# Kernel optimization log

Measured on AMD Instinct MI355X. Metric: run time of the kernel, lower is better.

The kernel has to match this reference:

```python
import jax, jax.numpy as jnp
import numpy as np

# --- config (Qwen3-Next linear attention defaults) ---
B, S, H = 1, 256, 2048
NK, NV, DK, DV, K = 4, 32, 128, 128, 4
KEY_DIM = NK * DK          # 512
VAL_DIM = NV * DV          # 4096
CONV_DIM = 2 * KEY_DIM + VAL_DIM  # 5120
EPS = 1e-6


def setup_inputs() -> dict:
    key = jax.random.key(0)
    ks = jax.random.split(key, 8)
    rn = lambda k, shape, sc: jax.random.normal(k, shape, jnp.float32) * sc
    return {
        "hidden_states": jax.random.normal(ks[0], (B, S, H), jnp.float32),
        "w_qkvz": rn(ks[1], (2 * KEY_DIM + 2 * VAL_DIM, H), 0.02),  # in_proj_qkvz weight
        "w_ba": rn(ks[2], (2 * NV, H), 0.02),                        # in_proj_ba weight
        "w_out": rn(ks[3], (H, VAL_DIM), 0.02),                      # out_proj weight
        "conv_w": rn(ks[4], (CONV_DIM, 1, K), 0.1),                  # depthwise conv weight [C,1,K]
        "dt_bias": jnp.ones((NV,), jnp.float32),
        "A_log": jnp.zeros((NV,), jnp.float32),
        "norm_w": jnp.ones((DV,), jnp.float32),
    }


def reference(hidden_states, w_qkvz, w_ba, w_out, conv_w, dt_bias, A_log, norm_w):
    b, s, _ = hidden_states.shape
    # input projections (Linear without bias: x @ W.T)
    qkvz = hidden_states @ w_qkvz.T                      # [B,S,9216]
    ba = hidden_states @ w_ba.T                          # [B,S,64]
    q, k, v, z = jnp.split(qkvz, [KEY_DIM, 2 * KEY_DIM, 2 * KEY_DIM + VAL_DIM], axis=-1)
    beta, alpha = jnp.split(ba, 2, axis=-1)              # each [B,S,NV]

    # causal depthwise conv over concat(q,k,v), then silu
    qkv = jnp.concatenate([q, k, v], axis=-1).transpose(0, 2, 1)   # [B,C,S]
    qkv = jax.lax.conv_general_dilated(
        qkv, conv_w, window_strides=(1,), padding=[(K - 1, 0)],
        dimension_numbers=("NCH", "OIH", "NCH"), feature_group_count=CONV_DIM)
    qkv = jax.nn.silu(qkv).transpose(0, 2, 1)            # [B,S,C]
    q, k, v = jnp.split(qkv, [KEY_DIM, 2 * KEY_DIM], axis=-1)

    q = q.reshape(b, s, NK, DK)
    k = k.reshape(b, s, NK, DK)
    v = v.reshape(b, s, NV, DV)
    z = z.reshape(b, s, NV, DV)

    # GQA-style head expansion (repeat_interleave)
    ratio = NV // NK
    q = jnp.repeat(q, ratio, axis=2)                     # [B,S,NV,DK]
    k = jnp.repeat(k, ratio, axis=2)

    # NOTE: original computes g = -softplus(-A_log - alpha) but never uses it (dead code).
    beta_g = jax.nn.sigmoid(beta + dt_bias)[..., None]   # [B,S,NV,1]
    q = q * (DK ** -0.5)

    # naive delta-rule: full outer-product tensor + cumsum (memory-bound)
    kv = jnp.einsum("bsnk,bsnv->bsnkv", k, v * beta_g)   # [B,S,NV,DK,DV]
    out = jnp.einsum("bsnk,bsnkv->bsnv", q, jnp.cumsum(kv, axis=1))  # [B,S,NV,DV]

    # gated RMSNorm over head_v_dim in fp32
    of = out.astype(jnp.float32)
    var = jnp.mean(of * of, axis=-1, keepdims=True)
    of = of * jax.lax.rsqrt(var + EPS) * norm_w
    of = of * jax.nn.silu(z.astype(jnp.float32))

    return of.reshape(b, s, VAL_DIM) @ w_out.T           # [B,S,H]
```

## Files before the change

kernel.cpp:

```cpp
#include <hip/hip_runtime.h>
#include <hip/hip_bf16.h>

#define S_LEN   256
#define HID     2048
#define NVH     32
#define DKD     128
#define DVD     128
#define KEYDIM  512
#define VALDIM  4096
#define CONVDIM 5120
#define QKVZ_N  9216
#define EPS_F   1e-6f

typedef __attribute__((ext_vector_type(8))) short bf16x8;
typedef __attribute__((ext_vector_type(4))) float f32x4;

__device__ __forceinline__ unsigned short f2bf(float f) {
    union { float f; unsigned int i; } v; v.f = f;
    unsigned int x = v.i;
    return (unsigned short)((x + 0x7FFFu + ((x >> 16) & 1u)) >> 16);
}
__device__ __forceinline__ unsigned int pk2(float x, float y) {
    union { __hip_bfloat162 h; unsigned int u; } c;
    c.h = __float22bfloat162_rn(float2{x, y});
    return c.u;
}
__device__ __forceinline__ bf16x8 pack_bf8(float4 lo, float4 hi) {
    union { uint4 u; bf16x8 h; } c;
    c.u.x = pk2(lo.x, lo.y); c.u.y = pk2(lo.z, lo.w);
    c.u.z = pk2(hi.x, hi.y); c.u.w = pk2(hi.z, hi.w);
    return c.h;
}
__device__ __forceinline__ void gl_lds16(const void* g, void* l) {
    __builtin_amdgcn_global_load_lds(
        (const __attribute__((address_space(1))) unsigned int*)g,
        (__attribute__((address_space(3))) unsigned int*)l,
        16, 0, 0);
}

template<int NT>
__global__ __launch_bounds__(256, 3)
void gemm_sn(const unsigned short* __restrict__ A, const float* __restrict__ B,
             float* __restrict__ Cpart, int N, int K, int kc) {
    __shared__ __align__(16) unsigned short As[256][64];
    __shared__ __align__(16) float Bs[NT][64];

    const int tid  = threadIdx.x;
    const int lane = tid & 63, wave = tid >> 6;
    const int quad = lane >> 4, l16 = lane & 15;
    const int n0 = blockIdx.x * NT;
    const int kbeg = blockIdx.y * kc;
    const int niter = kc >> 6;
    constexpr int NB = NT / 16;

    const int a_ro = lane >> 3;
    const int a_gc = (lane & 7) ^ a_ro;
    const int b_ro = lane >> 4;
    const int b_cs = lane & 15;

    f32x4 acc[4][NB];
#pragma unroll
    for (int i = 0; i < 4; i++)
#pragma unroll
        for (int j = 0; j < NB; j++) acc[i][j] = (f32x4){0.f, 0.f, 0.f, 0.f};

    auto stage = [&](int kk) {
#pragma unroll
        for (int t = 0; t < 8; ++t) {
            int rbase = wave * 64 + t * 8;
            gl_lds16(A + (size_t)(rbase + a_ro) * K + kk + a_gc * 8,
                     &As[rbase][0]);
        }
#pragma unroll
        for (int t = 0; t < NT / 16; ++t) {
            int rbase = wave * (NT / 4) + t * 4;
            int r = rbase + b_ro;
            int gc = b_cs ^ (r & 7);
            gl_lds16(B + (size_t)(n0 + r) * K + kk + gc * 4,
                     &Bs[rbase][0]);
        }
    };

    auto compute = [&]() {
#pragma unroll
        for (int ks = 0; ks < 2; ++ks) {
            bf16x8 af[4];
#pragma unroll
            for (int i = 0; i < 4; ++i) {
                int r = wave * 64 + i * 16 + l16;
                int c = (ks * 4 + quad) ^ (l16 & 7);
                af[i] = *(const bf16x8*)(&As[r][c * 8]);
            }
#pragma unroll
            for (int j = 0; j < NB; ++j) {
                int r = j * 16 + l16;
                int x = l16 & 7;
                int c0 = (ks * 8 + quad * 2) ^ x;
                int c1 = (ks * 8 + quad * 2 + 1) ^ x;
                float4 lo = *(const float4*)(&Bs[r][c0 * 4]);
                float4 hi = *(const float4*)(&Bs[r][c1 * 4]);
                bf16x8 bfr = pack_bf8(lo, hi);
#pragma unroll
                for (int i = 0; i < 4; ++i)
                    acc[i][j] = __builtin_amdgcn_mfma_f32_16x16x32_bf16(af[i], bfr, acc[i][j], 0, 0, 0);
            }
        }
    };

    stage(kbeg);
    for (int it = 0; it < niter; ++it) {
        __syncthreads();
        compute();
        if (it + 1 < niter) {
            __syncthreads();
            stage(kbeg + (it + 1) * 64);
        }
    }

    float* C = Cpart + (size_t)blockIdx.y * 256 * N;
#pragma unroll
    for (int i = 0; i < 4; i++)
#pragma unroll
        for (int j = 0; j < NB; j++)
#pragma unroll
            for (int r = 0; r < 4; r++) {
                int row = wave * 64 + i * 16 + quad * 4 + r;
                int col = n0 + j * 16 + l16;
                C[(size_t)row * N + col] = acc[i][j][r];
            }
}

__global__ __launch_bounds__(256)
void cvt_bf16(const float* __restrict__ in, unsigned short* __restrict__ out, int n8) {
    int i = blockIdx.x * 256 + threadIdx.x;
    if (i >= n8) return;
    const float4* p = (const float4*)in + (size_t)i * 2;
    float4 a = p[0], b = p[1];
    uint4 r;
    r.x = pk2(a.x, a.y); r.y = pk2(a.z, a.w);
    r.z = pk2(b.x, b.y); r.w = pk2(b.z, b.w);
    *((uint4*)out + i) = r;
}

template<int P>
__global__ void reduce_sum(const float* __restrict__ part, float* __restrict__ out, int n) {
    int i = (blockIdx.x * 256 + threadIdx.x) * 4;
    if (i >= n) return;
    float4 s = *(const float4*)(part + i);
#pragma unroll
    for (int p = 1; p < P; p++) {
        float4 v = *(const float4*)(part + (size_t)p * n + i);
        s.x += v.x; s.y += v.y; s.z += v.z; s.w += v.w;
    }
    *(float4*)(out + i) = s;
}

__global__ __launch_bounds__(256)
void ba_proj(const float* __restrict__ hs,
             const float* __restrict__ w_ba,
             float* __restrict__ ba) {
    int s = blockIdx.x;
    int n = threadIdx.x & 63, seg = threadIdx.x >> 6;
    const float* x = hs + (size_t)s * HID + seg * 512;
    const float* w = w_ba + (size_t)n * HID + seg * 512;
    float acc = 0.f;
#pragma unroll 4
    for (int k = 0; k < 512; k += 4) {
        float4 xv = *(const float4*)(x + k);
        float4 wv = *(const float4*)(w + k);
        acc += xv.x * wv.x + xv.y * wv.y + xv.z * wv.z + xv.w * wv.w;
    }
    __shared__ float parts[4][64];
    parts[seg][n] = acc;
    __syncthreads();
    if (threadIdx.x < 64)
        ba[s * 64 + threadIdx.x] = parts[0][threadIdx.x] + parts[1][threadIdx.x]
                                 + parts[2][threadIdx.x] + parts[3][threadIdx.x];
}

__global__ void conv_silu(const float* __restrict__ qkvz,
                          const float* __restrict__ conv_w,
                          float* __restrict__ out) {
    int idx = blockIdx.x * blockDim.x + threadIdx.x;
    if (idx >= S_LEN * CONVDIM) return;
    int s = idx / CONVDIM, c = idx % CONVDIM;
    float acc = 0.f;
#pragma unroll
    for (int j = 0; j < 4; j++) {
        int t = s - 3 + j;
        if (t >= 0) acc += qkvz[(size_t)t * QKVZ_N + c] * conv_w[c * 4 + j];
    }
    out[idx] = acc / (1.f + __expf(-acc));
}

__global__ __launch_bounds__(256)
void scores_k(const float* __restrict__ conv, const float* __restrict__ ba,
              const float* __restrict__ dt_bias, float* __restrict__ scores) {
    if (blockIdx.x > blockIdx.y) return;
    int hk = blockIdx.z;
    int s0 = blockIdx.y * 16, t0 = blockIdx.x * 16;
    __shared__ float Qs[16][132], Ks[16][132];
    int tid = threadIdx.x;
    int qoff = hk * DKD;
    int koff = KEYDIM + hk * DKD;
    for (int idx = tid; idx < 16 * 128; idx += 256) {
        int i = idx >> 7, d = idx & 127;
        Qs[i][d] = conv[(size_t)(s0 + i) * CONVDIM + qoff + d];
        Ks[i][d] = conv[(size_t)(t0 + i) * CONVDIM + koff + d];
    }
    __syncthreads();
    int tx = tid & 15, ty = tid >> 4;
    int s = s0 + ty, t = t0 + tx;
    float dot = 0.f;
    for (int d = 0; d < 128; d++) dot += Qs[ty][d] * Ks[tx][d];
    float base = (t <= s) ? dot * 0.08838834764831845f : 0.f;
#pragma unroll
    for (int v = 0; v < 8; v++) {
        int n = hk * 8 + v;
        float b = ba[t * 64 + n] + dt_bias[n];
        float bg = 1.f / (1.f + __expf(-b));
        scores[((size_t)n * 256 + s) * 256 + t] = base * bg;
    }
}

__global__ __launch_bounds__(256)
void attn_v(const float* __restrict__ scores, const float* __restrict__ conv,
            float* __restrict__ attn) {
    int n = blockIdx.y, s0 = blockIdx.x * 16;
    int voff = 2 * KEYDIM + n * DVD;
    __shared__ float Ss[16][17];
    __shared__ float Vs[16][132];
    int tid = threadIdx.x, sy = tid >> 4, dx = tid & 15;
    float acc[8] = {0.f, 0.f, 0.f, 0.f, 0.f, 0.f, 0.f, 0.f};
    for (int t0 = 0; t0 <= s0; t0 += 16) {
        Ss[sy][dx] = scores[((size_t)n * 256 + s0 + sy) * 256 + t0 + dx];
        const float* vp = conv + (size_t)(t0 + sy) * CONVDIM + voff + dx * 8;
        *(float4*)&Vs[sy][dx * 8]     = *(const float4*)vp;
        *(float4*)&Vs[sy][dx * 8 + 4] = *(const float4*)(vp + 4);
        __syncthreads();
#pragma unroll
        for (int j = 0; j < 16; j++) {
            float sv = Ss[sy][j];
#pragma unroll
            for (int r = 0; r < 8; r++) acc[r] += sv * Vs[j][dx + 16 * r];
        }
        __syncthreads();
    }
    float* op = attn + ((size_t)(s0 + sy) * NVH + n) * DVD;
#pragma unroll
    for (int r = 0; r < 8; r++) op[dx + 16 * r] = acc[r];
}

__global__ __launch_bounds__(128)
void rmsnorm_gate(const float* __restrict__ attn, const float* __restrict__ qkvz,
                  const float* __restrict__ norm_w,
                  unsigned short* __restrict__ normed) {
    int s = blockIdx.x >> 5, n = blockIdx.x & 31;
    int d = threadIdx.x;
    float x = attn[((size_t)s * NVH + n) * DVD + d];
    float sq = x * x;
#pragma unroll
    for (int off = 32; off > 0; off >>= 1) sq += __shfl_down(sq, off, 64);
    __shared__ float parts[2];
    if ((d & 63) == 0) parts[d >> 6] = sq;
    __syncthreads();
    float ms = (parts[0] + parts[1]) * (1.f / 128.f);
    float inv = rsqrtf(ms + EPS_F);
    float z = qkvz[(size_t)s * QKVZ_N + CONVDIM + n * DVD + d];
    float sz = z / (1.f + __expf(-z));
    float v = x * inv * norm_w[d] * sz;
    normed[((size_t)s * NVH + n) * DVD + d] = f2bf(v);
}

extern "C" void kernel_launch(void* const* d_in, const int* in_sizes, int n_in,
                              void* d_out, int out_size, void* d_ws, size_t ws_size,
                              hipStream_t stream) {
    const float* hs      = (const float*)d_in[0];
    const float* w_qkvz  = (const float*)d_in[1];
    const float* w_ba    = (const float*)d_in[2];
    const float* w_out   = (const float*)d_in[3];
    const float* conv_w  = (const float*)d_in[4];
    const float* dt_bias = (const float*)d_in[5];
    const float* norm_w  = (const float*)d_in[7];

    char* ws = (char*)d_ws;
    float* qkvz = (float*)ws;  ws += (size_t)S_LEN * QKVZ_N * 4;
    float* ba   = (float*)ws;  ws += (size_t)S_LEN * 64 * 4;
    float* conv = (float*)ws;  ws += (size_t)S_LEN * CONVDIM * 4;
    unsigned short* abf = (unsigned short*)ws;
    ws += (size_t)S_LEN * HID * 2;
    char* regB = ws;
    float* scratch1 = (float*)regB;
    unsigned short* normed = (unsigned short*)regB;
    float* scratch2 = (float*)(regB + 2097152);
    float* attn   = (float*)(regB + 2097152);
    float* scores = (float*)(regB + 2097152 + 4194304);

    const bool big = ws_size >= (size_t)55 * 1024 * 1024;
    const int sk1 = big ? 4 : 2;

    cvt_bf16<<<(S_LEN * HID / 8) / 256, 256, 0, stream>>>(hs, abf, S_LEN * HID / 8);
    if (big) gemm_sn<64><<<dim3(QKVZ_N / 64, 4), 256, 0, stream>>>(abf, w_qkvz, scratch1, QKVZ_N, HID, HID / 4);
    else     gemm_sn<64><<<dim3(QKVZ_N / 64, 2), 256, 0, stream>>>(abf, w_qkvz, scratch1, QKVZ_N, HID, HID / 2);
    ba_proj<<<S_LEN, 256, 0, stream>>>(hs, w_ba, ba);
    if (big) reduce_sum<4><<<(S_LEN * QKVZ_N) / 1024, 256, 0, stream>>>(scratch1, qkvz, S_LEN * QKVZ_N);
    else     reduce_sum<2><<<(S_LEN * QKVZ_N) / 1024, 256, 0, stream>>>(scratch1, qkvz, S_LEN * QKVZ_N);
    conv_silu<<<(S_LEN * CONVDIM) / 256, 256, 0, stream>>>(qkvz, conv_w, conv);
    scores_k<<<dim3(16, 16, 4), 256, 0, stream>>>(conv, ba, dt_bias, scores);
    attn_v<<<dim3(16, NVH), 256, 0, stream>>>(scores, conv, attn);
    rmsnorm_gate<<<S_LEN * NVH, 128, 0, stream>>>(attn, qkvz, norm_w, normed);
    gemm_sn<32><<<dim3(HID / 32, 8), 256, 0, stream>>>(normed, w_out, scratch2, HID, VALDIM, VALDIM / 8);
    reduce_sum<8><<<(S_LEN * HID) / 1024, 256, 0, stream>>>(scratch2, (float*)d_out, S_LEN * HID);
}
```

Baseline: 256.6 us.

## Double-buffer GEMM with M tiling and fuse reduce/conv and attn/rmsnorm kernels

The GEMM is rewritten to split M into two 128-row tiles on a 2x2 wave grid. It double-buffers LDS so the next K chunk is staged while the current one is computed, with a single barrier per iteration. The bf16 conversion of hidden_states is fused into ba_proj, the split-K reduction is fused with the causal conv+silu (z is also written out separately), and RMSNorm gating is fused into the attention-V epilogue. The aim is fewer launches, fewer full-size intermediate round trips and better load/compute overlap. The cost is higher LDS use and lower occupancy, and the split-K and workspace layout now depend on a changed ws_size threshold.

```diff
diff --git a/kernel.cpp b/kernel.cpp
--- a/kernel.cpp
+++ b/kernel.cpp
@@ -39,37 +39,37 @@
 }
 
 template<int NT>
-__global__ __launch_bounds__(256, 3)
-void gemm_sn(const unsigned short* __restrict__ A, const float* __restrict__ B,
+__global__ __launch_bounds__(256, 2)
+void gemm_db(const unsigned short* __restrict__ A, const float* __restrict__ B,
              float* __restrict__ Cpart, int N, int K, int kc) {
-    __shared__ __align__(16) unsigned short As[256][64];
-    __shared__ __align__(16) float Bs[NT][64];
+    __shared__ __align__(16) unsigned short As[2][128][64];
+    __shared__ __align__(16) float Bs[2][NT][64];
 
     const int tid  = threadIdx.x;
     const int lane = tid & 63, wave = tid >> 6;
+    const int wm = wave >> 1, wn = wave & 1;
     const int quad = lane >> 4, l16 = lane & 15;
-    const int n0 = blockIdx.x * NT;
-    const int kbeg = blockIdx.y * kc;
+    const int m0 = blockIdx.y * 128, n0 = blockIdx.x * NT;
+    const int kbeg = blockIdx.z * kc;
     const int niter = kc >> 6;
-    constexpr int NB = NT / 16;
 
     const int a_ro = lane >> 3;
     const int a_gc = (lane & 7) ^ a_ro;
     const int b_ro = lane >> 4;
     const int b_cs = lane & 15;
 
-    f32x4 acc[4][NB];
+    f32x4 acc[4][2];
 #pragma unroll
     for (int i = 0; i < 4; i++)
 #pragma unroll
-        for (int j = 0; j < NB; j++) acc[i][j] = (f32x4){0.f, 0.f, 0.f, 0.f};
-
-    auto stage = [&](int kk) {
-#pragma unroll
-        for (int t = 0; t < 8; ++t) {
-            int rbase = wave * 64 + t * 8;
-            gl_lds16(A + (size_t)(rbase + a_ro) * K + kk + a_gc * 8,
-                     &As[rbase][0]);
+        for (int j = 0; j < 2; j++) acc[i][j] = (f32x4){0.f, 0.f, 0.f, 0.f};
+
+    auto stage = [&](int buf, int kk) {
+#pragma unroll
+        for (int t = 0; t < 4; ++t) {
+            int rbase = wave * 32 + t * 8;
+            gl_lds16(A + (size_t)(m0 + rbase + a_ro) * K + kk + a_gc * 8,
+                     &As[buf][rbase][0]);
         }
 #pragma unroll
         for (int t = 0; t < NT / 16; ++t) {
@@ -77,28 +77,28 @@
             int r = rbase + b_ro;
             int gc = b_cs ^ (r & 7);
             gl_lds16(B + (size_t)(n0 + r) * K + kk + gc * 4,
-                     &Bs[rbase][0]);
+                     &Bs[buf][rbase][0]);
         }
     };
 
-    auto compute = [&]() {
+    auto compute = [&](int buf) {
 #pragma unroll
         for (int ks = 0; ks < 2; ++ks) {
             bf16x8 af[4];
 #pragma unroll
             for (int i = 0; i < 4; ++i) {
-                int r = wave * 64 + i * 16 + l16;
+                int r = wm * 64 + i * 16 + l16;
                 int c = (ks * 4 + quad) ^ (l16 & 7);
-                af[i] = *(const bf16x8*)(&As[r][c * 8]);
+                af[i] = *(const bf16x8*)(&As[buf][r][c * 8]);
             }
 #pragma unroll
-            for (int j = 0; j < NB; ++j) {
-                int r = j * 16 + l16;
+            for (int j = 0; j < 2; ++j) {
+                int r = wn * 32 + j * 16 + l16;
                 int x = l16 & 7;
                 int c0 = (ks * 8 + quad * 2) ^ x;
                 int c1 = (ks * 8 + quad * 2 + 1) ^ x;
-                float4 lo = *(const float4*)(&Bs[r][c0 * 4]);
-                float4 hi = *(const float4*)(&Bs[r][c1 * 4]);
+                float4 lo = *(const float4*)(&Bs[buf][r][c0 * 4]);
+                float4 hi = *(const float4*)(&Bs[buf][r][c1 * 4]);
                 bf16x8 bfr = pack_bf8(lo, hi);
 #pragma unroll
                 for (int i = 0; i < 4; ++i)
@@ -107,39 +107,25 @@
         }
     };
 
-    stage(kbeg);
+    stage(0, kbeg);
+    __syncthreads();
     for (int it = 0; it < niter; ++it) {
+        if (it + 1 < niter) stage((it + 1) & 1, kbeg + (it + 1) * 64);
+        compute(it & 1);
         __syncthreads();
-        compute();
-        if (it + 1 < niter) {
-            __syncthreads();
-            stage(kbeg + (it + 1) * 64);
-        }
-    }
-
-    float* C = Cpart + (size_t)blockIdx.y * 256 * N;
+    }
+
+    float* C = Cpart + (size_t)blockIdx.z * 256 * N;
 #pragma unroll
     for (int i = 0; i < 4; i++)
 #pragma unroll
-        for (int j = 0; j < NB; j++)
+        for (int j = 0; j < 2; j++)
 #pragma unroll
             for (int r = 0; r < 4; r++) {
-                int row = wave * 64 + i * 16 + quad * 4 + r;
-                int col = n0 + j * 16 + l16;
+                int row = m0 + wm * 64 + i * 16 + quad * 4 + r;
+                int col = n0 + wn * 32 + j * 16 + l16;
                 C[(size_t)row * N + col] = acc[i][j][r];
             }
-}
-
-__global__ __launch_bounds__(256)
-void cvt_bf16(const float* __restrict__ in, unsigned short* __restrict__ out, int n8) {
-    int i = blockIdx.x * 256 + threadIdx.x;
-    if (i >= n8) return;
-    const float4* p = (const float4*)in + (size_t)i * 2;
-    float4 a = p[0], b = p[1];
-    uint4 r;
-    r.x = pk2(a.x, a.y); r.y = pk2(a.z, a.w);
-    r.z = pk2(b.x, b.y); r.w = pk2(b.z, b.w);
-    *((uint4*)out + i) = r;
 }
 
 template<int P>
@@ -156,9 +142,8 @@
 }
 
 __global__ __launch_bounds__(256)
-void ba_proj(const float* __restrict__ hs,
-             const float* __restrict__ w_ba,
-             float* __restrict__ ba) {
+void ba_proj_cvt(const float* __restrict__ hs, const float* __restrict__ w_ba,
+                 float* __restrict__ ba, unsigned short* __restrict__ abf) {
     int s = blockIdx.x;
     int n = threadIdx.x & 63, seg = threadIdx.x >> 6;
     const float* x = hs + (size_t)s * HID + seg * 512;
@@ -172,25 +157,63 @@
     }
     __shared__ float parts[4][64];
     parts[seg][n] = acc;
+    {
+        int d = threadIdx.x * 8;
+        const float4* p = (const float4*)(hs + (size_t)s * HID + d);
+        float4 a = p[0], b = p[1];
+        uint4 r;
+        r.x = pk2(a.x, a.y); r.y = pk2(a.z, a.w);
+        r.z = pk2(b.x, b.y); r.w = pk2(b.z, b.w);
+        *(uint4*)(abf + (size_t)s * HID + d) = r;
+    }
     __syncthreads();
     if (threadIdx.x < 64)
         ba[s * 64 + threadIdx.x] = parts[0][threadIdx.x] + parts[1][threadIdx.x]
                                  + parts[2][threadIdx.x] + parts[3][threadIdx.x];
 }
 
-__global__ void conv_silu(const float* __restrict__ qkvz,
-                          const float* __restrict__ conv_w,
-                          float* __restrict__ out) {
-    int idx = blockIdx.x * blockDim.x + threadIdx.x;
-    if (idx >= S_LEN * CONVDIM) return;
-    int s = idx / CONVDIM, c = idx % CONVDIM;
-    float acc = 0.f;
-#pragma unroll
-    for (int j = 0; j < 4; j++) {
-        int t = s - 3 + j;
-        if (t >= 0) acc += qkvz[(size_t)t * QKVZ_N + c] * conv_w[c * 4 + j];
-    }
-    out[idx] = acc / (1.f + __expf(-acc));
+template<int P>
+__global__ __launch_bounds__(256)
+void sum_conv(const float* __restrict__ part, const float* __restrict__ conv_w,
+              float* __restrict__ conv, float* __restrict__ zs) {
+    const int s0 = blockIdx.y * 16;
+    const int c  = blockIdx.x * 1024 + threadIdx.x * 4;
+    auto sum4 = [&](int s) {
+        const float* p = part + (size_t)s * QKVZ_N + c;
+        float4 v = *(const float4*)p;
+#pragma unroll
+        for (int q = 1; q < P; q++) {
+            float4 w = *(const float4*)(p + (size_t)q * S_LEN * QKVZ_N);
+            v.x += w.x; v.y += w.y; v.z += w.z; v.w += w.w;
+        }
+        return v;
+    };
+    if (c < CONVDIM) {
+        float4 cw[4];
+#pragma unroll
+        for (int i = 0; i < 4; ++i) cw[i] = *(const float4*)(conv_w + (size_t)(c + i) * 4);
+        float4 w0{0,0,0,0}, w1{0,0,0,0}, w2{0,0,0,0};
+        for (int s = (s0 >= 3 ? s0 - 3 : 0); s < s0; ++s) { w0 = w1; w1 = w2; w2 = sum4(s); }
+        for (int s = s0; s < s0 + 16; ++s) {
+            float4 w3 = sum4(s);
+            float4 o;
+            o.x = w0.x * cw[0].x + w1.x * cw[0].y + w2.x * cw[0].z + w3.x * cw[0].w;
+            o.y = w0.y * cw[1].x + w1.y * cw[1].y + w2.y * cw[1].z + w3.y * cw[1].w;
+            o.z = w0.z * cw[2].x + w1.z * cw[2].y + w2.z * cw[2].z + w3.z * cw[2].w;
+            o.w = w0.w * cw[3].x + w1.w * cw[3].y + w2.w * cw[3].z + w3.w * cw[3].w;
+            o.x = o.x / (1.f + __expf(-o.x));
+            o.y = o.y / (1.f + __expf(-o.y));
+            o.z = o.z / (1.f + __expf(-o.z));
+            o.w = o.w / (1.f + __expf(-o.w));
+            *(float4*)(conv + (size_t)s * CONVDIM + c) = o;
+            w0 = w1; w1 = w2; w2 = w3;
+        }
+    } else {
+        for (int s = s0; s < s0 + 16; ++s) {
+            float4 v = sum4(s);
+            *(float4*)(zs + (size_t)s * VALDIM + (c - CONVDIM)) = v;
+        }
+    }
 }
 
 __global__ __launch_bounds__(256)
@@ -224,8 +247,9 @@
 }
 
 __global__ __launch_bounds__(256)
-void attn_v(const float* __restrict__ scores, const float* __restrict__ conv,
-            float* __restrict__ attn) {
+void attn_rms(const float* __restrict__ scores, const float* __restrict__ conv,
+              const float* __restrict__ zs, const float* __restrict__ norm_w,
+              unsigned short* __restrict__ normed) {
     int n = blockIdx.y, s0 = blockIdx.x * 16;
     int voff = 2 * KEYDIM + n * DVD;
     __shared__ float Ss[16][17];
@@ -246,30 +270,21 @@
         }
         __syncthreads();
     }
-    float* op = attn + ((size_t)(s0 + sy) * NVH + n) * DVD;
-#pragma unroll
-    for (int r = 0; r < 8; r++) op[dx + 16 * r] = acc[r];
-}
-
-__global__ __launch_bounds__(128)
-void rmsnorm_gate(const float* __restrict__ attn, const float* __restrict__ qkvz,
-                  const float* __restrict__ norm_w,
-                  unsigned short* __restrict__ normed) {
-    int s = blockIdx.x >> 5, n = blockIdx.x & 31;
-    int d = threadIdx.x;
-    float x = attn[((size_t)s * NVH + n) * DVD + d];
-    float sq = x * x;
-#pragma unroll
-    for (int off = 32; off > 0; off >>= 1) sq += __shfl_down(sq, off, 64);
-    __shared__ float parts[2];
-    if ((d & 63) == 0) parts[d >> 6] = sq;
-    __syncthreads();
-    float ms = (parts[0] + parts[1]) * (1.f / 128.f);
-    float inv = rsqrtf(ms + EPS_F);
-    float z = qkvz[(size_t)s * QKVZ_N + CONVDIM + n * DVD + d];
-    float sz = z / (1.f + __expf(-z));
-    float v = x * inv * norm_w[d] * sz;
-    normed[((size_t)s * NVH + n) * DVD + d] = f2bf(v);
+    float ssq = 0.f;
+#pragma unroll
+    for (int r = 0; r < 8; r++) ssq += acc[r] * acc[r];
+#pragma unroll
+    for (int m = 1; m <= 8; m <<= 1) ssq += __shfl_xor(ssq, m, 64);
+    float inv = rsqrtf(ssq * (1.f / 128.f) + EPS_F);
+    int s = s0 + sy;
+#pragma unroll
+    for (int r = 0; r < 8; r++) {
+        int d = dx + 16 * r;
+        float z = zs[(size_t)s * VALDIM + n * DVD + d];
+        float sz = z / (1.f + __expf(-z));
+        float v = acc[r] * inv * norm_w[d] * sz;
+        normed[((size_t)s * NVH + n) * DVD + d] = f2bf(v);
+    }
 }
 
 extern "C" void kernel_launch(void* const* d_in, const int* in_sizes, int n_in,
@@ -284,31 +299,26 @@
     const float* norm_w  = (const float*)d_in[7];
 
     char* ws = (char*)d_ws;
-    float* qkvz = (float*)ws;  ws += (size_t)S_LEN * QKVZ_N * 4;
+    unsigned short* abf = (unsigned short*)ws; ws += (size_t)S_LEN * HID * 2;
     float* ba   = (float*)ws;  ws += (size_t)S_LEN * 64 * 4;
     float* conv = (float*)ws;  ws += (size_t)S_LEN * CONVDIM * 4;
-    unsigned short* abf = (unsigned short*)ws;
-    ws += (size_t)S_LEN * HID * 2;
+    float* zs   = (float*)ws;  ws += (size_t)S_LEN * VALDIM * 4;
     char* regB = ws;
+    const bool big = ws_size >= (size_t)50 * 1024 * 1024;
+    const int sk1 = big ? 4 : 2;
+    const int sk2 = big ? 8 : 4;
     float* scratch1 = (float*)regB;
     unsigned short* normed = (unsigned short*)regB;
     float* scratch2 = (float*)(regB + 2097152);
-    float* attn   = (float*)(regB + 2097152);
-    float* scores = (float*)(regB + 2097152 + 4194304);
-
-    const bool big = ws_size >= (size_t)55 * 1024 * 1024;
-    const int sk1 = big ? 4 : 2;
-
-    cvt_bf16<<<(S_LEN * HID / 8) / 256, 256, 0, stream>>>(hs, abf, S_LEN * HID / 8);
-    if (big) gemm_sn<64><<<dim3(QKVZ_N / 64, 4), 256, 0, stream>>>(abf, w_qkvz, scratch1, QKVZ_N, HID, HID / 4);
-    else     gemm_sn<64><<<dim3(QKVZ_N / 64, 2), 256, 0, stream>>>(abf, w_qkvz, scratch1, QKVZ_N, HID, HID / 2);
-    ba_proj<<<S_LEN, 256, 0, stream>>>(hs, w_ba, ba);
-    if (big) reduce_sum<4><<<(S_LEN * QKVZ_N) / 1024, 256, 0, stream>>>(scratch1, qkvz, S_LEN * QKVZ_N);
-    else     reduce_sum<2><<<(S_LEN * QKVZ_N) / 1024, 256, 0, stream>>>(scratch1, qkvz, S_LEN * QKVZ_N);
-    conv_silu<<<(S_LEN * CONVDIM) / 256, 256, 0, stream>>>(qkvz, conv_w, conv);
+    float* scores   = (float*)(regB + 2097152 + (size_t)sk2 * 2097152);
+
+    ba_proj_cvt<<<S_LEN, 256, 0, stream>>>(hs, w_ba, ba, abf);
+    gemm_db<64><<<dim3(QKVZ_N / 64, 2, sk1), 256, 0, stream>>>(abf, w_qkvz, scratch1, QKVZ_N, HID, HID / sk1);
+    if (big) sum_conv<4><<<dim3(9, 16), 256, 0, stream>>>(scratch1, conv_w, conv, zs);
+    else     sum_conv<2><<<dim3(9, 16), 256, 0, stream>>>(scratch1, conv_w, conv, zs);
     scores_k<<<dim3(16, 16, 4), 256, 0, stream>>>(conv, ba, dt_bias, scores);
-    attn_v<<<dim3(16, NVH), 256, 0, stream>>>(scores, conv, attn);
-    rmsnorm_gate<<<S_LEN * NVH, 128, 0, stream>>>(attn, qkvz, norm_w, normed);
-    gemm_sn<32><<<dim3(HID / 32, 8), 256, 0, stream>>>(normed, w_out, scratch2, HID, VALDIM, VALDIM / 8);
-    reduce_sum<8><<<(S_LEN * HID) / 1024, 256, 0, stream>>>(scratch2, (float*)d_out, S_LEN * HID);
-}
+    attn_rms<<<dim3(16, NVH), 256, 0, stream>>>(scores, conv, zs, norm_w, normed);
+    gemm_db<64><<<dim3(HID / 64, 2, sk2), 256, 0, stream>>>(normed, w_out, scratch2, HID, VALDIM, VALDIM / sk2);
+    if (big) reduce_sum<8><<<(S_LEN * HID) / 1024, 256, 0, stream>>>(scratch2, (float*)d_out, S_LEN * HID);
+    else     reduce_sum<4><<<(S_LEN * HID) / 1024, 256, 0, stream>>>(scratch2, (float*)d_out, S_LEN * HID);
+}
```

New measurement: 244.7 us. -4.7%, faster.
